# Performance work log

Hardware: AMD Instinct MI355X
Metric: run time of the kernel (lower is better)

## Reference

```python
import jax, jax.numpy as jnp
import numpy as np

E, L, N_FEAT, N_NODES = 100000, 4, 20000, 20000
D, H = 64, 8
HD = H * D  # GRU hidden size = num_heads * out_dim
ALPHA = 0.001  # leaky relu slope


def setup_inputs() -> dict:
    key = jax.random.key(0)
    ks = jax.random.split(key, 8)
    s = 1.0 / np.sqrt(HD)
    return {
        "features": jax.random.normal(ks[0], (N_FEAT, D), jnp.float32),
        "edge_metapath_indices": jax.random.randint(ks[1], (E, L), 0, N_FEAT),
        "dst": jax.random.randint(ks[2], (E,), 0, N_NODES),
        "num_nodes": N_NODES,
        "w_ih": jax.random.uniform(ks[3], (3 * HD, D), jnp.float32, -s, s),
        "w_hh": jax.random.uniform(ks[4], (3 * HD, HD), jnp.float32, -s, s),
        "b_ih": jax.random.uniform(ks[5], (3 * HD,), jnp.float32, -s, s),
        "b_hh": jax.random.uniform(ks[6], (3 * HD,), jnp.float32, -s, s),
        "attn": jax.random.normal(ks[7], (H, D), jnp.float32) * 1.414 / np.sqrt(D),
    }


def _gru_last_hidden(x_seq, w_ih, w_hh, b_ih, b_hh):
    # x_seq: [L, E, D] -> final hidden [E, HD], torch GRU gate order (r, z, n)
    Eb = x_seq.shape[1]
    h0 = jnp.zeros((Eb, HD), x_seq.dtype)

    def step(h, x):
        gi = x @ w_ih.T + b_ih          # [E, 3*HD]
        gh = h @ w_hh.T + b_hh          # [E, 3*HD]
        ir, iz, inn = jnp.split(gi, 3, axis=-1)
        hr, hz, hn = jnp.split(gh, 3, axis=-1)
        r = jax.nn.sigmoid(ir + hr)
        z = jax.nn.sigmoid(iz + hz)
        n = jnp.tanh(inn + r * hn)
        h_new = (1.0 - z) * n + z * h
        return h_new, None

    h_last, _ = jax.lax.scan(step, h0, x_seq)
    return h_last


def reference(features, edge_metapath_indices, dst, num_nodes, w_ih, w_hh, b_ih, b_hh, attn):
    # edata: [E, L, D] gathered metapath node features
    edata = features[edge_metapath_indices]
    # GRU over metapath positions (torch permutes to seq-first)
    hidden = _gru_last_hidden(jnp.swapaxes(edata, 0, 1), w_ih, w_hh, b_ih, b_hh)  # [E, HD]
    eft = hidden.reshape(-1, H, D)                      # [E, H, D]
    # per-edge attention logits, leaky relu
    a = jax.nn.leaky_relu(jnp.einsum("ehd,hd->eh", eft, attn), ALPHA)  # [E, H]
    # edge softmax per destination node (segment softmax)
    amax = jax.ops.segment_max(a, dst, num_segments=num_nodes)         # [N, H]
    amax = jnp.where(jnp.isfinite(amax), amax, 0.0)
    a_exp = jnp.exp(a - amax[dst])
    denom = jax.ops.segment_sum(a_exp, dst, num_segments=num_nodes)    # [N, H]
    att = a_exp / jnp.maximum(denom[dst], 1e-12)                       # [E, H]
    # scatter-weighted sum of messages into destination nodes
    ft = jax.ops.segment_sum(eft * att[:, :, None], dst, num_segments=num_nodes)  # [N, H, D]
    return ft
```

## Files before the change

### kernel.cpp

```cpp
#include <hip/hip_runtime.h>
#include <cstdint>

typedef __attribute__((ext_vector_type(8))) short          bf16x8;
typedef __attribute__((ext_vector_type(8))) unsigned short u16x8;
typedef __attribute__((ext_vector_type(4))) float          f32x4;

__device__ __forceinline__ unsigned short f2bf(float x) {
    union { float f; unsigned u; } v; v.f = x;
    unsigned r = v.u + 0x7FFF + ((v.u >> 16) & 1);
    return (unsigned short)(r >> 16);
}
__device__ __forceinline__ float bf2f(unsigned short b) {
    union { float f; unsigned u; } v; v.u = ((unsigned)b) << 16;
    return v.f;
}

#define EB 64

__global__ __launch_bounds__(256) void conv_kernel(
    const float* __restrict__ feat, const float* __restrict__ w_ih,
    const float* __restrict__ w_hh,
    unsigned short* __restrict__ featb, unsigned short* __restrict__ wbi,
    unsigned short* __restrict__ wbh, int nfeat8)
{
    int t = blockIdx.x * 256 + threadIdx.x;
    if (t < nfeat8) {
        u16x8 o;
        #pragma unroll
        for (int i = 0; i < 8; ++i) o[i] = f2bf(feat[(size_t)t * 8 + i]);
        *(u16x8*)&featb[(size_t)t * 8] = o;
    } else if (t < nfeat8 + 98304) {
        int tt = t - nfeat8;
        int lane = tt & 63, q = tt >> 6;
        int jt = q >> 4, kb = q & 15;
        int j = jt * 16 + (lane & 15);
        int k0 = kb * 32 + (lane >> 4) * 8;
        u16x8 o;
        #pragma unroll
        for (int i = 0; i < 8; ++i) o[i] = f2bf(w_hh[(size_t)j * 512 + k0 + i]);
        *(u16x8*)&wbh[(size_t)tt * 8] = o;
    } else if (t < nfeat8 + 98304 + 12288) {
        int uu = t - nfeat8 - 98304;
        int lane = uu & 63, q = uu >> 6;
        int jt = q >> 1, kb = q & 1;
        int j = jt * 16 + (lane & 15);
        int k0 = kb * 32 + (lane >> 4) * 8;
        u16x8 o;
        #pragma unroll
        for (int i = 0; i < 8; ++i) o[i] = f2bf(w_ih[(size_t)j * 64 + k0 + i]);
        *(u16x8*)&wbi[(size_t)uu * 8] = o;
    }
}

__global__ __launch_bounds__(512, 4) void gru_mfma_kernel(
    const unsigned short* __restrict__ featb,
    const int* __restrict__ emi,
    const unsigned short* __restrict__ wbi,
    const unsigned short* __restrict__ wbh,
    const float* __restrict__ b_ih,
    const float* __restrict__ b_hh,
    float* __restrict__ eft,
    int E)
{
    __shared__ unsigned short hb[64 * 512];
    __shared__ unsigned short xb[64 * 64];

    const int tid  = threadIdx.x;
    const int lane = tid & 63;
    const int w    = tid >> 6;
    const int g    = lane >> 4;
    const int c    = lane & 15;
    const int e0   = blockIdx.x * EB;
    const f32x4 fzero = {0.f, 0.f, 0.f, 0.f};

    for (int l = 0; l < 4; ++l) {
        {
            int r = tid >> 3, p = tid & 7;
            int nidx = (e0 + r < E) ? emi[(e0 + r) * 4 + l] : 0;
            u16x8 v = *(const u16x8*)(featb + (size_t)nidx * 64 + p * 8);
            *(u16x8*)&xb[r * 64 + ((p * 8) ^ ((r & 7) << 3))] = v;
        }
        if (l > 0) {
            #pragma unroll
            for (int it = 0; it < 8; ++it) {
                int q = it * 512 + tid;
                int row = q >> 6, col8 = q & 63;
                const volatile unsigned* hsrc =
                    (const volatile unsigned*)((const char*)eft + (size_t)(e0 + row) * 2048) + (col8 << 2);
                unsigned u0 = hsrc[0], u1 = hsrc[1], u2 = hsrc[2], u3 = hsrc[3];
                uint4 v = {u0, u1, u2, u3};
                *(uint4*)&hb[row * 512 + (((col8 << 3)) ^ ((row & 7) << 3))] = v;
            }
        }
        __syncthreads();

        for (int cc = 0; cc < 4; ++cc) {
            const int j0 = (w << 6) + (cc << 4);
            const int jt = j0 >> 4;
            f32x4 ar[4], az[4], ain[4], ahn[4];
            #pragma unroll
            for (int m = 0; m < 4; ++m) { ar[m] = fzero; az[m] = fzero; ain[m] = fzero; ahn[m] = fzero; }

            #pragma unroll
            for (int kb = 0; kb < 2; ++kb) {
                bf16x8 br = *(const bf16x8*)(wbi + (((size_t)((jt     ) * 2 + kb)) * 64 + lane) * 8);
                bf16x8 bz = *(const bf16x8*)(wbi + (((size_t)((32 + jt) * 2 + kb)) * 64 + lane) * 8);
                bf16x8 bn = *(const bf16x8*)(wbi + (((size_t)((64 + jt) * 2 + kb)) * 64 + lane) * 8);
                #pragma unroll
                for (int m = 0; m < 4; ++m) {
                    int row = m * 16 + c;
                    bf16x8 a = *(const bf16x8*)&xb[row * 64 + ((kb * 32 + g * 8) ^ ((row & 7) << 3))];
                    ar[m]  = __builtin_amdgcn_mfma_f32_16x16x32_bf16(a, br, ar[m], 0, 0, 0);
                    az[m]  = __builtin_amdgcn_mfma_f32_16x16x32_bf16(a, bz, az[m], 0, 0, 0);
                    ain[m] = __builtin_amdgcn_mfma_f32_16x16x32_bf16(a, bn, ain[m], 0, 0, 0);
                }
            }
            if (l > 0) {
                #pragma unroll 2
                for (int kb = 0; kb < 16; ++kb) {
                    bf16x8 br = *(const bf16x8*)(wbh + (((size_t)((jt     ) * 16 + kb)) * 64 + lane) * 8);
                    bf16x8 bz = *(const bf16x8*)(wbh + (((size_t)((32 + jt) * 16 + kb)) * 64 + lane) * 8);
                    bf16x8 bn = *(const bf16x8*)(wbh + (((size_t)((64 + jt) * 16 + kb)) * 64 + lane) * 8);
                    #pragma unroll
                    for (int m = 0; m < 4; ++m) {
                        int row = m * 16 + c;
                        bf16x8 a = *(const bf16x8*)&hb[row * 512 + ((kb * 32 + g * 8) ^ ((row & 7) << 3))];
                        ar[m]  = __builtin_amdgcn_mfma_f32_16x16x32_bf16(a, br, ar[m], 0, 0, 0);
                        az[m]  = __builtin_amdgcn_mfma_f32_16x16x32_bf16(a, bz, az[m], 0, 0, 0);
                        ahn[m] = __builtin_amdgcn_mfma_f32_16x16x32_bf16(a, bn, ahn[m], 0, 0, 0);
                    }
                }
            }
            const int j = j0 + c;
            const float brr = b_ih[j] + b_hh[j];
            const float bzz = b_ih[512 + j] + b_hh[512 + j];
            const float bin = b_ih[1024 + j];
            const float bhn = b_hh[1024 + j];
            #pragma unroll
            for (int m = 0; m < 4; ++m) {
                #pragma unroll
                for (int q = 0; q < 4; ++q) {
                    int row = m * 16 + g * 4 + q;
                    float hold = (l > 0) ? bf2f(hb[row * 512 + (j ^ ((row & 7) << 3))]) : 0.f;
                    float r  = 1.f / (1.f + __expf(-(ar[m][q] + brr)));
                    float z  = 1.f / (1.f + __expf(-(az[m][q] + bzz)));
                    float pn = ain[m][q] + bin + r * (ahn[m][q] + bhn);
                    float ex = __expf(-2.f * pn);
                    float n  = (1.f - ex) / (1.f + ex);
                    float hnew = (1.f - z) * n + z * hold;
                    int e = e0 + row;
                    if (e < E) {
                        if (l < 3) {
                            unsigned short* hrow = (unsigned short*)((char*)eft + (size_t)e * 2048);
                            hrow[j] = f2bf(hnew);
                        } else {
                            eft[(size_t)e * 512 + j] = hnew;
                        }
                    }
                }
            }
        }
        __syncthreads();
    }
}

__global__ __launch_bounds__(256) void attn_kernel(
    const float* __restrict__ eft, const float* __restrict__ attn,
    const int* __restrict__ dst, float* __restrict__ aexp,
    float* __restrict__ denom, int E)
{
    int gidx = blockIdx.x * 256 + threadIdx.x;
    if (gidx >= E * 8) return;
    int e = gidx >> 3, h = gidx & 7;
    const float* fp = &eft[(size_t)e * 512 + (h << 6)];
    const float* ap = &attn[h << 6];
    float a = 0.f;
    #pragma unroll
    for (int k = 0; k < 16; ++k) {
        float4 f = *(const float4*)(fp + (k << 2));
        float4 wv = *(const float4*)(ap + (k << 2));
        a += f.x * wv.x + f.y * wv.y + f.z * wv.z + f.w * wv.w;
    }
    a = (a > 0.f) ? a : 0.001f * a;
    float ae = __expf(a);
    aexp[gidx] = ae;
    atomicAdd(&denom[(size_t)dst[e] * 8 + h], ae);
}

__global__ __launch_bounds__(256) void scatter_kernel(
    const float* __restrict__ eft, const float* __restrict__ aexp,
    const float* __restrict__ denom, const int* __restrict__ dst,
    float* __restrict__ out, long long total)
{
    long long gi = (long long)blockIdx.x * 256 + threadIdx.x;
    if (gi >= total) return;
    int e = (int)(gi >> 9);
    int j = (int)(gi & 511);
    int h = j >> 6;
    int n = dst[e];
    float wv = aexp[(size_t)e * 8 + h] / fmaxf(denom[(size_t)n * 8 + h], 1e-12f);
    atomicAdd(&out[(size_t)n * 512 + j], eft[gi] * wv);
}

extern "C" void kernel_launch(void* const* d_in, const int* in_sizes, int n_in,
                              void* d_out, int out_size, void* d_ws, size_t ws_size,
                              hipStream_t stream)
{
    const float* feat = (const float*)d_in[0];
    const int*   emi  = (const int*)d_in[1];
    const int*   dst  = (const int*)d_in[2];
    const float* w_ih = (const float*)d_in[4];
    const float* w_hh = (const float*)d_in[5];
    const float* b_ih = (const float*)d_in[6];
    const float* b_hh = (const float*)d_in[7];
    const float* attn = (const float*)d_in[8];

    const int E = in_sizes[1] / 4;
    const int N = out_size / 512;
    const int nfeat8 = in_sizes[0] / 8;

    float* eft = (float*)d_ws;
    unsigned short* featb = (unsigned short*)(eft + (size_t)E * 512);
    unsigned short* wbi   = featb + (size_t)(in_sizes[0]);
    unsigned short* wbh   = wbi + (size_t)96 * 2 * 64 * 8;
    float* aexp  = (float*)featb;
    float* denom = aexp + (size_t)E * 8;
    float* out   = (float*)d_out;

    int conv_total = nfeat8 + 98304 + 12288;
    conv_kernel<<<(conv_total + 255) / 256, 256, 0, stream>>>(
        feat, w_ih, w_hh, featb, wbi, wbh, nfeat8);

    gru_mfma_kernel<<<(E + EB - 1) / EB, 512, 0, stream>>>(
        featb, emi, wbi, wbh, b_ih, b_hh, eft, E);

    (void)hipMemsetAsync(denom, 0, (size_t)N * 8 * sizeof(float), stream);
    (void)hipMemsetAsync(d_out, 0, (size_t)out_size * sizeof(float), stream);

    attn_kernel<<<(E * 8 + 255) / 256, 256, 0, stream>>>(eft, attn, dst, aexp, denom, E);

    long long total = (long long)E * 512;
    scatter_kernel<<<(int)((total + 255) / 256), 256, 0, stream>>>(
        eft, aexp, denom, dst, out, total);
}
```

Before: 1.784 ms.

## Keep GRU hidden state in double-buffered LDS instead of global round-trip

The intermediate bf16 hidden state is now kept in a ping-pong pair of shared-memory buffers between timesteps, so it is no longer written to and re-read from global memory through volatile loads. The hidden-weight loads are software-prefetched two k-steps ahead and the input-projection loop is fully unrolled. LDS use doubles to about 136 KB per block and the launch bound drops to 2 blocks, which lowers occupancy and adds register pressure from the prefetch buffers.

```diff
diff --git a/kernel.cpp b/kernel.cpp
--- a/kernel.cpp
+++ b/kernel.cpp
@@ -15,7 +15,8 @@
     return v.f;
 }
 
-#define EB 64
+#define EB   64
+#define NTHR 512
 
 __global__ __launch_bounds__(256) void conv_kernel(
     const float* __restrict__ feat, const float* __restrict__ w_ih,
@@ -52,7 +53,7 @@
     }
 }
 
-__global__ __launch_bounds__(512, 4) void gru_mfma_kernel(
+__global__ __launch_bounds__(NTHR, 2) void gru_mfma_kernel(
     const unsigned short* __restrict__ featb,
     const int* __restrict__ emi,
     const unsigned short* __restrict__ wbi,
@@ -62,8 +63,8 @@
     float* __restrict__ eft,
     int E)
 {
-    __shared__ unsigned short hb[64 * 512];
-    __shared__ unsigned short xb[64 * 64];
+    __shared__ unsigned short hb[2][EB * 512];
+    __shared__ unsigned short xb[EB * 64];
 
     const int tid  = threadIdx.x;
     const int lane = tid & 63;
@@ -74,24 +75,14 @@
     const f32x4 fzero = {0.f, 0.f, 0.f, 0.f};
 
     for (int l = 0; l < 4; ++l) {
+        const int rbuf = (l + 1) & 1;
+        const int wbuf = l & 1;
         {
             int r = tid >> 3, p = tid & 7;
             int nidx = (e0 + r < E) ? emi[(e0 + r) * 4 + l] : 0;
             u16x8 v = *(const u16x8*)(featb + (size_t)nidx * 64 + p * 8);
             *(u16x8*)&xb[r * 64 + ((p * 8) ^ ((r & 7) << 3))] = v;
         }
-        if (l > 0) {
-            #pragma unroll
-            for (int it = 0; it < 8; ++it) {
-                int q = it * 512 + tid;
-                int row = q >> 6, col8 = q & 63;
-                const volatile unsigned* hsrc =
-                    (const volatile unsigned*)((const char*)eft + (size_t)(e0 + row) * 2048) + (col8 << 2);
-                unsigned u0 = hsrc[0], u1 = hsrc[1], u2 = hsrc[2], u3 = hsrc[3];
-                uint4 v = {u0, u1, u2, u3};
-                *(uint4*)&hb[row * 512 + (((col8 << 3)) ^ ((row & 7) << 3))] = v;
-            }
-        }
         __syncthreads();
 
         for (int cc = 0; cc < 4; ++cc) {
@@ -101,30 +92,48 @@
             #pragma unroll
             for (int m = 0; m < 4; ++m) { ar[m] = fzero; az[m] = fzero; ain[m] = fzero; ahn[m] = fzero; }
 
-            #pragma unroll
-            for (int kb = 0; kb < 2; ++kb) {
-                bf16x8 br = *(const bf16x8*)(wbi + (((size_t)((jt     ) * 2 + kb)) * 64 + lane) * 8);
-                bf16x8 bz = *(const bf16x8*)(wbi + (((size_t)((32 + jt) * 2 + kb)) * 64 + lane) * 8);
-                bf16x8 bn = *(const bf16x8*)(wbi + (((size_t)((64 + jt) * 2 + kb)) * 64 + lane) * 8);
+            {
+                bf16x8 r0 = *(const bf16x8*)(wbi + (((size_t)((jt     ) * 2 + 0)) * 64 + lane) * 8);
+                bf16x8 r1 = *(const bf16x8*)(wbi + (((size_t)((jt     ) * 2 + 1)) * 64 + lane) * 8);
+                bf16x8 z0 = *(const bf16x8*)(wbi + (((size_t)((32 + jt) * 2 + 0)) * 64 + lane) * 8);
+                bf16x8 z1 = *(const bf16x8*)(wbi + (((size_t)((32 + jt) * 2 + 1)) * 64 + lane) * 8);
+                bf16x8 n0 = *(const bf16x8*)(wbi + (((size_t)((64 + jt) * 2 + 0)) * 64 + lane) * 8);
+                bf16x8 n1 = *(const bf16x8*)(wbi + (((size_t)((64 + jt) * 2 + 1)) * 64 + lane) * 8);
                 #pragma unroll
                 for (int m = 0; m < 4; ++m) {
                     int row = m * 16 + c;
-                    bf16x8 a = *(const bf16x8*)&xb[row * 64 + ((kb * 32 + g * 8) ^ ((row & 7) << 3))];
-                    ar[m]  = __builtin_amdgcn_mfma_f32_16x16x32_bf16(a, br, ar[m], 0, 0, 0);
-                    az[m]  = __builtin_amdgcn_mfma_f32_16x16x32_bf16(a, bz, az[m], 0, 0, 0);
-                    ain[m] = __builtin_amdgcn_mfma_f32_16x16x32_bf16(a, bn, ain[m], 0, 0, 0);
+                    bf16x8 a0 = *(const bf16x8*)&xb[row * 64 + ((g * 8) ^ ((row & 7) << 3))];
+                    ar[m]  = __builtin_amdgcn_mfma_f32_16x16x32_bf16(a0, r0, ar[m], 0, 0, 0);
+                    az[m]  = __builtin_amdgcn_mfma_f32_16x16x32_bf16(a0, z0, az[m], 0, 0, 0);
+                    ain[m] = __builtin_amdgcn_mfma_f32_16x16x32_bf16(a0, n0, ain[m], 0, 0, 0);
+                    bf16x8 a1 = *(const bf16x8*)&xb[row * 64 + ((32 + g * 8) ^ ((row & 7) << 3))];
+                    ar[m]  = __builtin_amdgcn_mfma_f32_16x16x32_bf16(a1, r1, ar[m], 0, 0, 0);
+                    az[m]  = __builtin_amdgcn_mfma_f32_16x16x32_bf16(a1, z1, az[m], 0, 0, 0);
+                    ain[m] = __builtin_amdgcn_mfma_f32_16x16x32_bf16(a1, n1, ain[m], 0, 0, 0);
                 }
             }
             if (l > 0) {
-                #pragma unroll 2
+                const unsigned short* hrow = &hb[rbuf][0];
+                bf16x8 pr[2], pz[2], pn[2];
+                pr[0] = *(const bf16x8*)(wbh + (((size_t)((jt     ) * 16 + 0)) * 64 + lane) * 8);
+                pr[1] = *(const bf16x8*)(wbh + (((size_t)((jt     ) * 16 + 1)) * 64 + lane) * 8);
+                pz[0] = *(const bf16x8*)(wbh + (((size_t)((32 + jt) * 16 + 0)) * 64 + lane) * 8);
+                pz[1] = *(const bf16x8*)(wbh + (((size_t)((32 + jt) * 16 + 1)) * 64 + lane) * 8);
+                pn[0] = *(const bf16x8*)(wbh + (((size_t)((64 + jt) * 16 + 0)) * 64 + lane) * 8);
+                pn[1] = *(const bf16x8*)(wbh + (((size_t)((64 + jt) * 16 + 1)) * 64 + lane) * 8);
+                #pragma unroll
                 for (int kb = 0; kb < 16; ++kb) {
-                    bf16x8 br = *(const bf16x8*)(wbh + (((size_t)((jt     ) * 16 + kb)) * 64 + lane) * 8);
-                    bf16x8 bz = *(const bf16x8*)(wbh + (((size_t)((32 + jt) * 16 + kb)) * 64 + lane) * 8);
-                    bf16x8 bn = *(const bf16x8*)(wbh + (((size_t)((64 + jt) * 16 + kb)) * 64 + lane) * 8);
+                    const int cur = kb & 1;
+                    bf16x8 br = pr[cur], bz = pz[cur], bn = pn[cur];
+                    if (kb + 2 < 16) {
+                        pr[cur] = *(const bf16x8*)(wbh + (((size_t)((jt     ) * 16 + kb + 2)) * 64 + lane) * 8);
+                        pz[cur] = *(const bf16x8*)(wbh + (((size_t)((32 + jt) * 16 + kb + 2)) * 64 + lane) * 8);
+                        pn[cur] = *(const bf16x8*)(wbh + (((size_t)((64 + jt) * 16 + kb + 2)) * 64 + lane) * 8);
+                    }
                     #pragma unroll
                     for (int m = 0; m < 4; ++m) {
                         int row = m * 16 + c;
-                        bf16x8 a = *(const bf16x8*)&hb[row * 512 + ((kb * 32 + g * 8) ^ ((row & 7) << 3))];
+                        bf16x8 a = *(const bf16x8*)&hrow[row * 512 + ((kb * 32 + g * 8) ^ ((row & 7) << 3))];
                         ar[m]  = __builtin_amdgcn_mfma_f32_16x16x32_bf16(a, br, ar[m], 0, 0, 0);
                         az[m]  = __builtin_amdgcn_mfma_f32_16x16x32_bf16(a, bz, az[m], 0, 0, 0);
                         ahn[m] = __builtin_amdgcn_mfma_f32_16x16x32_bf16(a, bn, ahn[m], 0, 0, 0);
@@ -141,21 +150,18 @@
                 #pragma unroll
                 for (int q = 0; q < 4; ++q) {
                     int row = m * 16 + g * 4 + q;
-                    float hold = (l > 0) ? bf2f(hb[row * 512 + (j ^ ((row & 7) << 3))]) : 0.f;
+                    float hold = (l > 0) ? bf2f(hb[rbuf][row * 512 + (j ^ ((row & 7) << 3))]) : 0.f;
                     float r  = 1.f / (1.f + __expf(-(ar[m][q] + brr)));
                     float z  = 1.f / (1.f + __expf(-(az[m][q] + bzz)));
-                    float pn = ain[m][q] + bin + r * (ahn[m][q] + bhn);
-                    float ex = __expf(-2.f * pn);
+                    float pn2 = ain[m][q] + bin + r * (ahn[m][q] + bhn);
+                    float ex = __expf(-2.f * pn2);
                     float n  = (1.f - ex) / (1.f + ex);
                     float hnew = (1.f - z) * n + z * hold;
-                    int e = e0 + row;
-                    if (e < E) {
-                        if (l < 3) {
-                            unsigned short* hrow = (unsigned short*)((char*)eft + (size_t)e * 2048);
-                            hrow[j] = f2bf(hnew);
-                        } else {
-                            eft[(size_t)e * 512 + j] = hnew;
-                        }
+                    if (l < 3) {
+                        hb[wbuf][row * 512 + (j ^ ((row & 7) << 3))] = f2bf(hnew);
+                    } else {
+                        int e = e0 + row;
+                        if (e < E) eft[(size_t)e * 512 + j] = hnew;
                     }
                 }
             }
@@ -231,7 +237,7 @@
     conv_kernel<<<(conv_total + 255) / 256, 256, 0, stream>>>(
         feat, w_ih, w_hh, featb, wbi, wbh, nfeat8);
 
-    gru_mfma_kernel<<<(E + EB - 1) / EB, 512, 0, stream>>>(
+    gru_mfma_kernel<<<(E + EB - 1) / EB, NTHR, 0, stream>>>(
         featb, emi, wbi, wbh, b_ih, b_hh, eft, E);
 
     (void)hipMemsetAsync(denom, 0, (size_t)N * 8 * sizeof(float), stream);
```

New measurement: 1.509 ms. 1.18x faster.
